# Kernel optimization log

Measured on AMD Instinct MI355X. Metric: run time of the kernel, lower is better.

Reference implementation:

```python
import jax, jax.numpy as jnp
import numpy as np

LEAKY_ALPHA = 0.2

def setup_inputs() -> dict:
    key = jax.random.key(0)
    kA, kH, kW, k1, k2 = jax.random.split(key, 5)
    B, N, F_in, D = 8, 2048, 256, 128
    return {
        "A": jax.random.normal(kA, (B, N, N), dtype=jnp.float32),
        "H": jax.random.normal(kH, (B, N, F_in), dtype=jnp.float32),
        "W": jax.random.normal(kW, (F_in, D), dtype=jnp.float32) * 0.05,
        "a_1": jax.random.normal(k1, (D, 1), dtype=jnp.float32) * 0.05,
        "a_2": jax.random.normal(k2, (D, 1), dtype=jnp.float32) * 0.05,
    }

def reference(A, H, W, a_1, a_2):
    # H_: [B, N, D] node projections
    H_ = jnp.einsum('bnf,fd->bnd', H, W)
    # additive attention logits: f1[b,i] + f2[b,j] -> [B, N, N]
    f1 = H_ @ a_1            # [B, N, 1]
    f2 = H_ @ a_2            # [B, N, 1]
    e = jax.nn.leaky_relu(f1 + jnp.swapaxes(f2, 1, 2), negative_slope=LEAKY_ALPHA)
    # NOTE: original multiplies logits by the binary adjacency (not -inf masking)
    mask = (A > 0.0).astype(jnp.float32)
    alpha = jax.nn.softmax(e * mask, axis=-1)   # [B, N, N]
    H_next = jnp.matmul(alpha, H_)              # [B, N, D]
    return H_next
```

## Files before the change

### kernel.cpp

```cpp
#include <hip/hip_runtime.h>


#define LEAKY 0.2f
constexpr int Bb = 8, Nn = 2048, FIN = 256, Dd = 128;
constexpr int NROW = Bb * Nn;
constexpr int RS = 132;
constexpr float LOG2E = 1.44269504088896f;

typedef __attribute__((ext_vector_type(8))) short short8;
typedef __attribute__((ext_vector_type(4))) float float4v;

__device__ __forceinline__ unsigned short f2bf(float f) {
    union { float f; unsigned int i; } v; v.f = f;
    return (unsigned short)((v.i + 0x8000u) >> 16);
}

__device__ __forceinline__ void stage_read(const float* __restrict__ base, int rstride,
                                           int tid, float4* st) {
    const int row = tid >> 4, c16 = tid & 15;
    const float* p = base + (size_t)row * rstride + c16 * 4;
    #pragma unroll
    for (int k = 0; k < 4; ++k) st[k] = *(const float4*)(p + 64 * k);
}
__device__ __forceinline__ void stage_write(float* __restrict__ As, int tid, const float4* st) {
    const int row = tid >> 4, c16 = tid & 15, sw = row & 7;
    float* dst = As + row * 256;
    #pragma unroll
    for (int k = 0; k < 4; ++k) {
        const int col = 4 * (c16 + 16 * k);
        dst[(col + 0) ^ sw] = st[k].x;
        dst[(col + 1) ^ sw] = st[k].y;
        dst[(col + 2) ^ sw] = st[k].z;
        dst[(col + 3) ^ sw] = st[k].w;
    }
}

__global__ __launch_bounds__(256) void prep_wf(const float* __restrict__ W,
                                               unsigned short* __restrict__ Wf) {
    int idx = blockIdx.x * 256 + threadIdx.x;
    int k = idx >> 7, d = idx & 127;
    Wf[(size_t)((k >> 3) * 128 + d) * 8 + (k & 7)] = f2bf(W[idx]);
}

__global__ __launch_bounds__(256) void proj_kernel(
    const float* __restrict__ Hg,
    const unsigned short* __restrict__ Wf,
    const float* __restrict__ a1, const float* __restrict__ a2,
    unsigned short* __restrict__ Hbt2,
    float* __restrict__ f1g, float* __restrict__ f2g) {
    __shared__ float Rbuf[4 * 16 * RS];
    __shared__ float Hs[4096];

    const int tid = threadIdx.x;
    const int w = tid >> 6, lane = tid & 63, q = lane >> 4, m = lane & 15;
    const int row0 = blockIdx.x * 16;

    float4 st[4];
    stage_read(Hg + (size_t)row0 * FIN, FIN, tid, st);
    stage_write(Hs, tid, st);
    __syncthreads();

    float4v acc[8] = {};
    const float* arow = Hs + m * 256;
    const int sw = m & 7;
    #pragma unroll
    for (int c = 0; c < 2; ++c) {
        const int cb = w * 64 + 32 * c + 8 * q;
        union { short8 v; unsigned short us[8]; } Af;
        #pragma unroll
        for (int j = 0; j < 8; ++j) Af.us[j] = f2bf(arow[cb + (j ^ sw)]);
        #pragma unroll
        for (int t = 0; t < 8; ++t) {
            const short8 bfr = *(const short8*)(Wf + (size_t)((8 * w + 4 * c + q) * 128 + 16 * t + m) * 8);
            acc[t] = __builtin_amdgcn_mfma_f32_16x16x32_bf16(Af.v, bfr, acc[t], 0, 0, 0);
        }
    }
    #pragma unroll
    for (int t = 0; t < 8; ++t)
        #pragma unroll
        for (int rg = 0; rg < 4; ++rg)
            Rbuf[w * 16 * RS + (4 * q + rg) * RS + 16 * t + m] = acc[t][rg];
    __syncthreads();

    const int row = tid >> 4, c4 = tid & 15;
    float o[8];
    #pragma unroll
    for (int half = 0; half < 2; ++half) {
        const int col = 64 * half + 4 * c4;
        const float* rb = Rbuf + row * RS + col;
        float4 s0 = *(const float4*)(rb);
        float4 s1 = *(const float4*)(rb + 16 * RS);
        float4 s2 = *(const float4*)(rb + 32 * RS);
        float4 s3 = *(const float4*)(rb + 48 * RS);
        o[4 * half + 0] = s0.x + s1.x + s2.x + s3.x;
        o[4 * half + 1] = s0.y + s1.y + s2.y + s3.y;
        o[4 * half + 2] = s0.z + s1.z + s2.z + s3.z;
        o[4 * half + 3] = s0.w + s1.w + s2.w + s3.w;
    }
    {
        float4 A1a = *(const float4*)(a1 + 4 * c4), A1b = *(const float4*)(a1 + 64 + 4 * c4);
        float4 A2a = *(const float4*)(a2 + 4 * c4), A2b = *(const float4*)(a2 + 64 + 4 * c4);
        float p1 = o[0]*A1a.x + o[1]*A1a.y + o[2]*A1a.z + o[3]*A1a.w
                 + o[4]*A1b.x + o[5]*A1b.y + o[6]*A1b.z + o[7]*A1b.w;
        float p2 = o[0]*A2a.x + o[1]*A2a.y + o[2]*A2a.z + o[3]*A2a.w
                 + o[4]*A2b.x + o[5]*A2b.y + o[6]*A2b.z + o[7]*A2b.w;
        #pragma unroll
        for (int off = 1; off <= 8; off <<= 1) {
            p1 += __shfl_xor(p1, off, 16);
            p2 += __shfl_xor(p2, off, 16);
        }
        if (c4 == 0) { f1g[row0 + row] = p1 * LOG2E; f2g[row0 + row] = p2 * LOG2E; }
    }
    *(float4*)(Rbuf + row * RS + 4 * c4)      = make_float4(o[0], o[1], o[2], o[3]);
    *(float4*)(Rbuf + row * RS + 64 + 4 * c4) = make_float4(o[4], o[5], o[6], o[7]);
    __syncthreads();
    const int d = tid >> 1, h = tid & 1;
    union { uint4 v; unsigned short us[8]; } oP;
    #pragma unroll
    for (int r = 0; r < 8; ++r) oP.us[r] = f2bf(Rbuf[(8 * h + r) * RS + d]);
    *(uint4*)(Hbt2 + (size_t)((2 * blockIdx.x + h) * 128 + d) * 8) = oP.v;
}

__global__ __launch_bounds__(256) void attn_kernel(
    const float* __restrict__ Ag,
    const unsigned short* __restrict__ Hbt2,
    const float* __restrict__ f1g, const float* __restrict__ f2g,
    float* __restrict__ Og) {
    __shared__ float Rbuf[4 * 16 * RS];

    const int tid = threadIdx.x;
    const int w = tid >> 6, lane = tid & 63, q = lane >> 4, m = lane & 15;
    const int b = blockIdx.y, i0 = blockIdx.x * 16;
    const size_t bRow = (size_t)b * Nn;

    const float fi = f1g[bRow + i0 + m];
    const float* Arow = Ag + (bRow + i0 + m) * (size_t)Nn + 512 * w;
    const float* f2w  = f2g + bRow + 512 * w;
    const unsigned short* Hb = Hbt2 + bRow * 128;
    const int g0w = 64 * w;

    short8 ones;
    #pragma unroll
    for (int k = 0; k < 8; ++k) ones[k] = (short)0x3F80;

    float4v acc[8] = {};
    float4v accl = {};

    float4 av[2][4];
    float f2r[2];

    #pragma unroll
    for (int c = 0; c < 2; ++c) {
        av[0][2 * c]     = *(const float4*)(Arow + 32 * c + 8 * q);
        av[0][2 * c + 1] = *(const float4*)(Arow + 32 * c + 8 * q + 4);
    }
    f2r[0] = f2w[lane];

    #pragma unroll
    for (int s = 0; s < 8; ++s) {
        const int p = s & 1;
        const unsigned short* bg = Hb + (size_t)(g0w + 8 * s) * 1024;
        short8 bf[16];
        #pragma unroll
        for (int t = 0; t < 8; ++t) {
            bf[2 * t]     = *(const short8*)(bg + ((size_t)(q    ) * 128 + 16 * t + m) * 8);
            bf[2 * t + 1] = *(const short8*)(bg + ((size_t)(q + 4) * 128 + 16 * t + m) * 8);
        }
        __builtin_amdgcn_sched_barrier(0);
        if (s < 7) {
            #pragma unroll
            for (int c = 0; c < 2; ++c) {
                av[p ^ 1][2 * c]     = *(const float4*)(Arow + 64 * (s + 1) + 32 * c + 8 * q);
                av[p ^ 1][2 * c + 1] = *(const float4*)(Arow + 64 * (s + 1) + 32 * c + 8 * q + 4);
            }
            f2r[p ^ 1] = f2w[64 * (s + 1) + lane];
        }
        __builtin_amdgcn_sched_barrier(0);
        short8 pa[2];
        #pragma unroll
        for (int c = 0; c < 2; ++c) {
            union { short8 v; unsigned int u[4]; } P;
            #pragma unroll
            for (int k = 0; k < 4; ++k) {
                float pv[2];
                #pragma unroll
                for (int hh = 0; hh < 2; ++hh) {
                    const int j = 2 * k + hh;
                    const float a  = ((const float*)&av[p][2 * c + (j >> 2)])[j & 3];
                    const float s2 = fi + __shfl(f2r[p], 32 * c + 8 * q + j, 64);
                    const float t2 = fmaxf(s2, LEAKY * s2);
                    float e;
                    asm("v_exp_f32 %0, %1" : "=v"(e) : "v"(t2));
                    pv[hh] = (a > 0.f) ? e : 1.0f;
                }
                asm("v_cvt_pk_bf16_f32 %0, %1, %2" : "=v"(P.u[k]) : "v"(pv[0]), "v"(pv[1]));
            }
            pa[c] = P.v;
        }
        #pragma unroll
        for (int t = 0; t < 8; ++t) {
            acc[t] = __builtin_amdgcn_mfma_f32_16x16x32_bf16(pa[0], bf[2 * t],     acc[t], 0, 0, 0);
            acc[t] = __builtin_amdgcn_mfma_f32_16x16x32_bf16(pa[1], bf[2 * t + 1], acc[t], 0, 0, 0);
        }
        accl = __builtin_amdgcn_mfma_f32_16x16x32_bf16(pa[0], ones, accl, 0, 0, 0);
        accl = __builtin_amdgcn_mfma_f32_16x16x32_bf16(pa[1], ones, accl, 0, 0, 0);
    }

    #pragma unroll
    for (int t = 0; t < 8; ++t)
        #pragma unroll
        for (int rg = 0; rg < 4; ++rg)
            Rbuf[w * 16 * RS + (4 * q + rg) * RS + 16 * t + m] = acc[t][rg];
    if (m == 0) {
        #pragma unroll
        for (int rg = 0; rg < 4; ++rg)
            Rbuf[w * 16 * RS + (4 * q + rg) * RS + 128] = accl[rg];
    }
    __syncthreads();

    const int row = tid >> 4, c4 = tid & 15;
    const float l = Rbuf[row * RS + 128] + Rbuf[16 * RS + row * RS + 128]
                  + Rbuf[32 * RS + row * RS + 128] + Rbuf[48 * RS + row * RS + 128];
    const float rl = 1.0f / l;
    float* orow = Og + (bRow + i0 + row) * (size_t)Dd;
    #pragma unroll
    for (int half = 0; half < 2; ++half) {
        const int col = 64 * half + 4 * c4;
        const float* rb = Rbuf + row * RS + col;
        float4 s0 = *(const float4*)(rb);
        float4 s1 = *(const float4*)(rb + 16 * RS);
        float4 s2 = *(const float4*)(rb + 32 * RS);
        float4 s3 = *(const float4*)(rb + 48 * RS);
        float4 o;
        o.x = (s0.x + s1.x + s2.x + s3.x) * rl;
        o.y = (s0.y + s1.y + s2.y + s3.y) * rl;
        o.z = (s0.z + s1.z + s2.z + s3.z) * rl;
        o.w = (s0.w + s1.w + s2.w + s3.w) * rl;
        *(float4*)(orow + col) = o;
    }
}

extern "C" void kernel_launch(void* const* d_in, const int* in_sizes, int n_in,
                              void* d_out, int out_size, void* d_ws, size_t ws_size,
                              hipStream_t stream) {
    const float* A  = (const float*)d_in[0];
    const float* H  = (const float*)d_in[1];
    const float* W  = (const float*)d_in[2];
    const float* a1 = (const float*)d_in[3];
    const float* a2 = (const float*)d_in[4];
    float* out = (float*)d_out;

    unsigned short* Wf   = (unsigned short*)d_ws;
    unsigned short* Hbt2 = Wf + FIN * Dd;
    float* f1 = (float*)(Hbt2 + (size_t)Dd * NROW);
    float* f2 = f1 + NROW;

    prep_wf<<<dim3(FIN * Dd / 256), 256, 0, stream>>>(W, Wf);
    proj_kernel<<<dim3(NROW / 16), 256, 0, stream>>>(H, Wf, a1, a2, Hbt2, f1, f2);
    attn_kernel<<<dim3(Nn / 16, Bb), 256, 0, stream>>>(A, Hbt2, f1, f2, out);
}
```

Baseline: 227.2 us.

## Precompute adjacency bitmask in a separate kernel and feed attention with bits

```diff
diff --git a/kernel.cpp b/kernel.cpp
--- a/kernel.cpp
+++ b/kernel.cpp
@@ -40,6 +40,24 @@
     int idx = blockIdx.x * 256 + threadIdx.x;
     int k = idx >> 7, d = idx & 127;
     Wf[(size_t)((k >> 3) * 128 + d) * 8 + (k & 7)] = f2bf(W[idx]);
+}
+
+__global__ __launch_bounds__(256) void prep_mask(const float* __restrict__ A,
+                                                 unsigned short* __restrict__ Mg) {
+    const size_t t = (size_t)blockIdx.x * 256 + threadIdx.x;
+    const float4* p = (const float4*)(A + t * 16);
+    float4 v[4];
+    #pragma unroll
+    for (int k = 0; k < 4; ++k) v[k] = p[k];
+    unsigned m = 0;
+    #pragma unroll
+    for (int k = 0; k < 4; ++k) {
+        const float* f = (const float*)&v[k];
+        #pragma unroll
+        for (int j = 0; j < 4; ++j)
+            if (f[j] > 0.f) m |= 1u << (4 * k + j);
+    }
+    Mg[t] = (unsigned short)m;
 }
 
 __global__ __launch_bounds__(256) void proj_kernel(
@@ -122,7 +140,7 @@
 }
 
 __global__ __launch_bounds__(256) void attn_kernel(
-    const float* __restrict__ Ag,
+    const unsigned short* __restrict__ Mg,
     const unsigned short* __restrict__ Hbt2,
     const float* __restrict__ f1g, const float* __restrict__ f2g,
     float* __restrict__ Og) {
@@ -134,11 +152,20 @@
     const size_t bRow = (size_t)b * Nn;
 
     const float fi = f1g[bRow + i0 + m];
-    const float* Arow = Ag + (bRow + i0 + m) * (size_t)Nn + 512 * w;
-    const float* f2w  = f2g + bRow + 512 * w;
+    const unsigned short* Mrow = Mg + (bRow + i0 + m) * 128 + 32 * w + q;
+    const float* f2w = f2g + bRow + 512 * w;
     const unsigned short* Hb = Hbt2 + bRow * 128;
     const int g0w = 64 * w;
 
+    int msk[8];
+    float f2r[8];
+    #pragma unroll
+    for (int s = 0; s < 8; ++s) {
+        msk[s] = Mrow[4 * s];
+        f2r[s] = f2w[64 * s + lane];
+    }
+    const int vq = q << 6;
+
     short8 ones;
     #pragma unroll
     for (int k = 0; k < 8; ++k) ones[k] = (short)0x3F80;
@@ -146,36 +173,16 @@
     float4v acc[8] = {};
     float4v accl = {};
 
-    float4 av[2][4];
-    float f2r[2];
-
-    #pragma unroll
-    for (int c = 0; c < 2; ++c) {
-        av[0][2 * c]     = *(const float4*)(Arow + 32 * c + 8 * q);
-        av[0][2 * c + 1] = *(const float4*)(Arow + 32 * c + 8 * q + 4);
-    }
-    f2r[0] = f2w[lane];
-
     #pragma unroll
     for (int s = 0; s < 8; ++s) {
-        const int p = s & 1;
+        __builtin_amdgcn_sched_barrier(0);
         const unsigned short* bg = Hb + (size_t)(g0w + 8 * s) * 1024;
         short8 bf[16];
         #pragma unroll
         for (int t = 0; t < 8; ++t) {
-            bf[2 * t]     = *(const short8*)(bg + ((size_t)(q    ) * 128 + 16 * t + m) * 8);
-            bf[2 * t + 1] = *(const short8*)(bg + ((size_t)(q + 4) * 128 + 16 * t + m) * 8);
-        }
-        __builtin_amdgcn_sched_barrier(0);
-        if (s < 7) {
-            #pragma unroll
-            for (int c = 0; c < 2; ++c) {
-                av[p ^ 1][2 * c]     = *(const float4*)(Arow + 64 * (s + 1) + 32 * c + 8 * q);
-                av[p ^ 1][2 * c + 1] = *(const float4*)(Arow + 64 * (s + 1) + 32 * c + 8 * q + 4);
-            }
-            f2r[p ^ 1] = f2w[64 * (s + 1) + lane];
-        }
-        __builtin_amdgcn_sched_barrier(0);
+            bf[2 * t]     = *(const short8*)(bg + ((size_t)(2 * q)     * 128 + 16 * t + m) * 8);
+            bf[2 * t + 1] = *(const short8*)(bg + ((size_t)(2 * q + 1) * 128 + 16 * t + m) * 8);
+        }
         short8 pa[2];
         #pragma unroll
         for (int c = 0; c < 2; ++c) {
@@ -185,13 +192,14 @@
                 float pv[2];
                 #pragma unroll
                 for (int hh = 0; hh < 2; ++hh) {
-                    const int j = 2 * k + hh;
-                    const float a  = ((const float*)&av[p][2 * c + (j >> 2)])[j & 3];
-                    const float s2 = fi + __shfl(f2r[p], 32 * c + 8 * q + j, 64);
+                    const int jj = 2 * k + hh;
+                    const int f2i = __builtin_amdgcn_ds_bpermute(vq + 4 * (8 * c + jj),
+                                                                 __float_as_int(f2r[s]));
+                    const float s2 = fi + __int_as_float(f2i);
                     const float t2 = fmaxf(s2, LEAKY * s2);
                     float e;
                     asm("v_exp_f32 %0, %1" : "=v"(e) : "v"(t2));
-                    pv[hh] = (a > 0.f) ? e : 1.0f;
+                    pv[hh] = (msk[s] & (1 << (8 * c + jj))) ? e : 1.0f;
                 }
                 asm("v_cvt_pk_bf16_f32 %0, %1, %2" : "=v"(P.u[k]) : "v"(pv[0]), "v"(pv[1]));
             }
@@ -254,8 +262,10 @@
     unsigned short* Hbt2 = Wf + FIN * Dd;
     float* f1 = (float*)(Hbt2 + (size_t)Dd * NROW);
     float* f2 = f1 + NROW;
+    unsigned short* Mg = (unsigned short*)(f2 + NROW);
 
     prep_wf<<<dim3(FIN * Dd / 256), 256, 0, stream>>>(W, Wf);
+    prep_mask<<<dim3((NROW * (size_t)Nn / 16) / 256), 256, 0, stream>>>(A, Mg);
     proj_kernel<<<dim3(NROW / 16), 256, 0, stream>>>(H, Wf, a1, a2, Hbt2, f1, f2);
-    attn_kernel<<<dim3(Nn / 16, Bb), 256, 0, stream>>>(A, Hbt2, f1, f2, out);
-}
+    attn_kernel<<<dim3(Nn / 16, Bb), 256, 0, stream>>>(Mg, Hbt2, f1, f2, out);
+}
```

After: 239.8 us. 1.06x slower.

## Stage adjacency via coalesced block loads into LDS byte masks with double buffering

Applied to the files above, without the earlier changes.

```diff
diff --git a/kernel.cpp b/kernel.cpp
--- a/kernel.cpp
+++ b/kernel.cpp
@@ -5,6 +5,7 @@
 constexpr int Bb = 8, Nn = 2048, FIN = 256, Dd = 128;
 constexpr int NROW = Bb * Nn;
 constexpr int RS = 132;
+constexpr int MSTRIDE = 68;
 constexpr float LOG2E = 1.44269504088896f;
 
 typedef __attribute__((ext_vector_type(8))) short short8;
@@ -32,6 +33,19 @@
         dst[(col + 1) ^ sw] = st[k].y;
         dst[(col + 2) ^ sw] = st[k].z;
         dst[(col + 3) ^ sw] = st[k].w;
+    }
+}
+__device__ __forceinline__ void mask_write(unsigned* __restrict__ Ms, int tid, const float4* st) {
+    const int row = tid >> 4, c16 = tid & 15;
+    unsigned* dst = Ms + MSTRIDE * row + c16;
+    #pragma unroll
+    for (int k = 0; k < 4; ++k) {
+        const float4 v = st[k];
+        unsigned dw = (v.x > 0.f ? 0x000000FFu : 0u)
+                    | (v.y > 0.f ? 0x0000FF00u : 0u)
+                    | (v.z > 0.f ? 0x00FF0000u : 0u)
+                    | (v.w > 0.f ? 0xFF000000u : 0u);
+        dst[16 * k] = dw;
     }
 }
 
@@ -126,7 +140,8 @@
     const unsigned short* __restrict__ Hbt2,
     const float* __restrict__ f1g, const float* __restrict__ f2g,
     float* __restrict__ Og) {
-    __shared__ float Rbuf[4 * 16 * RS];
+    __shared__ float smem[8448];
+    unsigned* Msk = (unsigned*)smem;
 
     const int tid = threadIdx.x;
     const int w = tid >> 6, lane = tid & 63, q = lane >> 4, m = lane & 15;
@@ -134,10 +149,10 @@
     const size_t bRow = (size_t)b * Nn;
 
     const float fi = f1g[bRow + i0 + m];
-    const float* Arow = Ag + (bRow + i0 + m) * (size_t)Nn + 512 * w;
-    const float* f2w  = f2g + bRow + 512 * w;
-    const unsigned short* Hb = Hbt2 + bRow * 128;
-    const int g0w = 64 * w;
+    const float* Abase = Ag + (bRow + i0) * (size_t)Nn;
+    const float* f2p = f2g + bRow;
+    const unsigned short* Bb2 = Hbt2 + bRow * 128;
+    const int jw = w * 64;
 
     short8 ones;
     #pragma unroll
@@ -145,40 +160,36 @@
 
     float4v acc[8] = {};
     float4v accl = {};
-
-    float4 av[2][4];
-    float f2r[2];
-
-    #pragma unroll
-    for (int c = 0; c < 2; ++c) {
-        av[0][2 * c]     = *(const float4*)(Arow + 32 * c + 8 * q);
-        av[0][2 * c + 1] = *(const float4*)(Arow + 32 * c + 8 * q + 4);
-    }
-    f2r[0] = f2w[lane];
-
-    #pragma unroll
-    for (int s = 0; s < 8; ++s) {
-        const int p = s & 1;
-        const unsigned short* bg = Hb + (size_t)(g0w + 8 * s) * 1024;
+    float4 st[4];
+
+    stage_read(Abase, Nn, tid, st);
+    mask_write(Msk, tid, st);
+
+    for (int ch = 0; ch < 8; ++ch) {
+        __syncthreads();
+        const int jt = ch * 256;
+        const unsigned* Ms = Msk + (ch & 1) * (16 * MSTRIDE);
+        const unsigned short* bg = Bb2 + (size_t)((jt + jw) >> 3) * 1024;
         short8 bf[16];
         #pragma unroll
         for (int t = 0; t < 8; ++t) {
             bf[2 * t]     = *(const short8*)(bg + ((size_t)(q    ) * 128 + 16 * t + m) * 8);
             bf[2 * t + 1] = *(const short8*)(bg + ((size_t)(q + 4) * 128 + 16 * t + m) * 8);
         }
+        float4 f2v[2][2];
+        #pragma unroll
+        for (int c = 0; c < 2; ++c) {
+            const float* fp = f2p + jt + jw + 32 * c + 8 * q;
+            f2v[c][0] = *(const float4*)(fp);
+            f2v[c][1] = *(const float4*)(fp + 4);
+        }
         __builtin_amdgcn_sched_barrier(0);
-        if (s < 7) {
-            #pragma unroll
-            for (int c = 0; c < 2; ++c) {
-                av[p ^ 1][2 * c]     = *(const float4*)(Arow + 64 * (s + 1) + 32 * c + 8 * q);
-                av[p ^ 1][2 * c + 1] = *(const float4*)(Arow + 64 * (s + 1) + 32 * c + 8 * q + 4);
-            }
-            f2r[p ^ 1] = f2w[64 * (s + 1) + lane];
-        }
+        if (ch < 7) stage_read(Abase + jt + 256, Nn, tid, st);
         __builtin_amdgcn_sched_barrier(0);
         short8 pa[2];
         #pragma unroll
         for (int c = 0; c < 2; ++c) {
+            const uint2 md = *(const uint2*)(Ms + MSTRIDE * m + 16 * w + 8 * c + 2 * q);
             union { short8 v; unsigned int u[4]; } P;
             #pragma unroll
             for (int k = 0; k < 4; ++k) {
@@ -186,12 +197,13 @@
                 #pragma unroll
                 for (int hh = 0; hh < 2; ++hh) {
                     const int j = 2 * k + hh;
-                    const float a  = ((const float*)&av[p][2 * c + (j >> 2)])[j & 3];
-                    const float s2 = fi + __shfl(f2r[p], 32 * c + 8 * q + j, 64);
+                    const unsigned dw = (j < 4) ? md.x : md.y;
+                    const int m32 = ((int)(dw << (24 - 8 * (j & 3)))) >> 24;
+                    const float s2 = fi + ((const float*)&f2v[c][j >> 2])[j & 3];
                     const float t2 = fmaxf(s2, LEAKY * s2);
                     float e;
                     asm("v_exp_f32 %0, %1" : "=v"(e) : "v"(t2));
-                    pv[hh] = (a > 0.f) ? e : 1.0f;
+                    pv[hh] = __int_as_float((m32 & __float_as_int(e)) | (~m32 & 0x3F800000));
                 }
                 asm("v_cvt_pk_bf16_f32 %0, %1, %2" : "=v"(P.u[k]) : "v"(pv[0]), "v"(pv[1]));
             }
@@ -204,8 +216,11 @@
         }
         accl = __builtin_amdgcn_mfma_f32_16x16x32_bf16(pa[0], ones, accl, 0, 0, 0);
         accl = __builtin_amdgcn_mfma_f32_16x16x32_bf16(pa[1], ones, accl, 0, 0, 0);
-    }
-
+        if (ch < 7) mask_write(Msk + ((ch + 1) & 1) * (16 * MSTRIDE), tid, st);
+    }
+
+    __syncthreads();
+    float* Rbuf = smem;
     #pragma unroll
     for (int t = 0; t < 8; ++t)
         #pragma unroll
```

New measurement: 222.1 us. 2.3% less time.
